# Kernel optimization log

Hardware: AMD Instinct MI355X
Metric: run time of the kernel (lower is better)

The kernel has to match this reference:

```python
import jax, jax.numpy as jnp
import numpy as np

B, N, D, H = 256, 64, 128, 64

def _w(key, shape, fan_in):
    return jax.random.normal(key, shape, jnp.float32) * (1.0 / np.sqrt(fan_in))

def setup_inputs() -> dict:
    key = jax.random.key(0)
    ks = jax.random.split(key, 6)
    return {
        "observations": jax.random.normal(ks[0], (B, N, D), jnp.float32),
        "enc_w": _w(ks[1], (D, H), D), "enc_b": jnp.zeros((H,), jnp.float32),
        "gate_w1": _w(ks[2], (2 * H, H), 2 * H), "gate_b1": jnp.zeros((H,), jnp.float32),
        "gate_w2": _w(ks[3], (H, 1), H), "gate_b2": jnp.zeros((1,), jnp.float32),
        "msg_w1": _w(ks[4], (H, H), H), "msg_b1": jnp.zeros((H,), jnp.float32),
        "msg_w2": _w(ks[5], (H, H), H), "msg_b2": jnp.zeros((H,), jnp.float32),
    }

def reference(observations, enc_w, enc_b, gate_w1, gate_b1, gate_w2, gate_b2,
              msg_w1, msg_b1, msg_w2, msg_b2):
    # encoder: (B, N, H)
    enc = jax.nn.relu(observations @ enc_w + enc_b)
    h = enc.shape[-1]
    # gate layer 1 on concat([e_i, e_j]) == e_i @ W_top + e_j @ W_bot; avoids
    # materializing the (B, N, N, 2H) concat tensor.
    w_i, w_j = gate_w1[:h], gate_w1[h:]
    gi = enc @ w_i                       # (B, N, H) contribution of receiver i
    gj = enc @ w_j + gate_b1             # (B, N, H) contribution of sender j
    hid = jax.nn.relu(gi[:, :, None, :] + gj[:, None, :, :])   # (B, N, N, H)
    gates = jax.nn.sigmoid(jnp.squeeze(hid @ gate_w2, -1) + gate_b2[0])  # (B, N, N)
    # message_gen(encoded): identical for every i in the original loop
    msg = jax.nn.relu(enc @ msg_w1 + msg_b1) @ msg_w2 + msg_b2  # (B, N, H)
    # enhanced[b, i] = sum_j gates[b, i, j] * msg[b, j]
    enhanced = jnp.einsum('bij,bjh->bih', gates, msg)           # (B, N, H)
    return enhanced
```

## Files before the change

### kernel.cpp

```cpp
#include <hip/hip_runtime.h>

typedef float  f32x4  __attribute__((ext_vector_type(4)));
typedef short  bf16x8 __attribute__((ext_vector_type(8)));

#define Bb 256

__device__ __forceinline__ uint cvtpk(float lo, float hi) {
    uint r;
    asm("v_cvt_pk_bf16_f32 %0, %1, %2" : "=v"(r) : "v"(lo), "v"(hi));
    return r;
}
__device__ __forceinline__ ushort f2b1(float v) { return (ushort)cvtpk(v, v); }

__device__ __forceinline__ void gl_lds16(const void* g, void* l) {
    __builtin_amdgcn_global_load_lds(
        (const __attribute__((address_space(1))) unsigned int*)g,
        (__attribute__((address_space(3))) unsigned int*)l, 16, 0, 0);
}

union U8 { uint u[4]; bf16x8 v; };

__global__ __launch_bounds__(256) void gcm_prep(
    const float* __restrict__ obs, const float* __restrict__ enc_w,
    const float* __restrict__ gate_w1, const float* __restrict__ msg_w1,
    const float* __restrict__ msg_w2,
    ushort* __restrict__ obs_bf, ushort* __restrict__ wimg)
{
    const int bid = blockIdx.x, t = threadIdx.x;
    if (bid < 1024) {
        const int G  = bid * 256 + t;
        const int e0 = G * 8;
        const int b  = e0 >> 13;
        const int r  = (e0 >> 7) & 63;
        const int d0 = e0 & 127;
        const int ds = d0 ^ ((r & 7) << 3);
        const float* src = obs + (((size_t)b * 64 + r) * 128 + ds);
        float4 f0 = *(const float4*)src;
        float4 f1 = *(const float4*)(src + 4);
        uint4 o;
        o.x = cvtpk(f0.x, f0.y); o.y = cvtpk(f0.z, f0.w);
        o.z = cvtpk(f1.x, f1.y); o.w = cvtpk(f1.z, f1.w);
        *(uint4*)(obs_bf + e0) = o;
    } else {
        const int G  = (bid - 1024) * 256 + t;
        const int e0 = G * 8;
        float v[8];
        if (e0 < 8192) {
            const int n  = e0 >> 7;
            const int k0 = (e0 & 127) ^ ((n & 7) << 3);
            #pragma unroll
            for (int j = 0; j < 8; ++j) v[j] = enc_w[(k0 + j) * 64 + n];
        } else {
            const int e  = e0 - 8192;
            const int n  = e >> 6;
            const int k0 = (e & 63) ^ ((n & 7) << 3);
            const float* base; int col;
            if (n < 64)       { base = gate_w1;           col = n;       }
            else if (n < 128) { base = gate_w1 + 64 * 64; col = n - 64;  }
            else if (n < 192) { base = msg_w1;            col = n - 128; }
            else              { base = msg_w2;            col = n - 192; }
            #pragma unroll
            for (int j = 0; j < 8; ++j) v[j] = base[(k0 + j) * 64 + col];
        }
        uint4 o;
        o.x = cvtpk(v[0], v[1]); o.y = cvtpk(v[2], v[3]);
        o.z = cvtpk(v[4], v[5]); o.w = cvtpk(v[6], v[7]);
        *(uint4*)(wimg + e0) = o;
    }
}

__global__ __launch_bounds__(1024, 1) void gcm_main(
    const ushort* __restrict__ obs_bf, const ushort* __restrict__ wimg,
    const float* __restrict__ enc_b, const float* __restrict__ gate_b1,
    const float* __restrict__ gate_w2, const float* __restrict__ gate_b2,
    const float* __restrict__ msg_b1, const float* __restrict__ msg_b2,
    float* __restrict__ out)
{
    const int bb   = blockIdx.x;
    const int t    = threadIdx.x;
    const int lane = t & 63;
    const int wv   = t >> 6;
    const int lr   = lane & 15;
    const int lg   = lane >> 4;
    const int rt   = wv & 3;
    const int ct   = wv >> 2;

    __shared__ __align__(16) char arena[131072];
    ushort* s_obs    = (ushort*)(arena);
    ushort* s_encwT  = (ushort*)(arena + 16384);
    ushort* s_wT     = (ushort*)(arena + 32768);
    ushort* s_enc    = (ushort*)(arena + 65536);
    ushort* s_msgh   = (ushort*)(arena + 73728);
    float*  s_gi     = (float*) (arena + 81920);
    float*  s_gj     = (float*) (arena + 98304);
    ushort* s_msgT   = (ushort*)(arena + 114688);
    ushort* s_gatesb = (ushort*)(arena + 122880);

    {
        const ushort* ob = obs_bf + (size_t)bb * 8192 + wv * 512 + lane * 8;
        gl_lds16(ob, arena + wv * 1024);
        const ushort* ew = wimg + wv * 512 + lane * 8;
        gl_lds16(ew, arena + 16384 + wv * 1024);
        const ushort* w0 = wimg + 8192 + wv * 512 + lane * 8;
        gl_lds16(w0, arena + 32768 + wv * 1024);
        const ushort* w1 = wimg + 8192 + (wv + 16) * 512 + lane * 8;
        gl_lds16(w1, arena + 32768 + (wv + 16) * 1024);
    }
    __syncthreads();

    {
        f32x4 acc = (f32x4){0.f, 0.f, 0.f, 0.f};
        const int arow = rt * 16 + lr;
        const int n = ct * 16 + lr;
        #pragma unroll
        for (int ks = 0; ks < 4; ++ks) {
            const int k0 = ks * 32 + lg * 8;
            bf16x8 a  = *(const bf16x8*)(s_obs + ((arow * 128 + k0) ^ ((arow & 7) << 3)));
            bf16x8 bf = *(const bf16x8*)(s_encwT + ((n * 128 + k0) ^ ((n & 7) << 3)));
            acc = __builtin_amdgcn_mfma_f32_16x16x32_bf16(a, bf, acc, 0, 0, 0);
        }
        const float be = enc_b[n];
        float v0 = fmaxf(acc[0] + be, 0.f), v1 = fmaxf(acc[1] + be, 0.f);
        float v2 = fmaxf(acc[2] + be, 0.f), v3 = fmaxf(acc[3] + be, 0.f);
        uint pA = cvtpk(v0, v1), pB = cvtpk(v2, v3);
        const int rb = rt * 16 + lg * 4;
        s_enc[((rb + 0) * 64 + n) ^ (((rb + 0) & 7) << 3)] = (ushort)pA;
        s_enc[((rb + 1) * 64 + n) ^ (((rb + 1) & 7) << 3)] = (ushort)(pA >> 16);
        s_enc[((rb + 2) * 64 + n) ^ (((rb + 2) & 7) << 3)] = (ushort)pB;
        s_enc[((rb + 3) * 64 + n) ^ (((rb + 3) & 7) << 3)] = (ushort)(pB >> 16);
    }
    __syncthreads();

    {
        f32x4 acc[3];
        #pragma unroll
        for (int q = 0; q < 3; ++q) acc[q] = (f32x4){0.f, 0.f, 0.f, 0.f};
        const int arow = rt * 16 + lr;
        #pragma unroll
        for (int ks = 0; ks < 2; ++ks) {
            const int k0 = ks * 32 + lg * 8;
            bf16x8 a = *(const bf16x8*)(s_enc + ((arow * 64 + k0) ^ ((arow & 7) << 3)));
            #pragma unroll
            for (int q = 0; q < 3; ++q) {
                const int n = (ct * 3 + q) * 16 + lr;
                bf16x8 bf = *(const bf16x8*)(s_wT + ((n * 64 + k0) ^ ((n & 7) << 3)));
                acc[q] = __builtin_amdgcn_mfma_f32_16x16x32_bf16(a, bf, acc[q], 0, 0, 0);
            }
        }
        const int rb = rt * 16 + lg * 4;
        #pragma unroll
        for (int q = 0; q < 3; ++q) {
            const int nfull = (ct * 3 + q) * 16;
            const int cc = nfull + lr;
            if (nfull < 64) {
                #pragma unroll
                for (int rr = 0; rr < 4; ++rr) {
                    const int row = rb + rr;
                    s_gi[(row * 64 + cc) ^ ((row & 7) << 2)] = acc[q][rr];
                }
            } else if (nfull < 128) {
                const float b1 = gate_b1[cc - 64];
                #pragma unroll
                for (int rr = 0; rr < 4; ++rr) {
                    const int row = rb + rr;
                    s_gj[(row * 64 + (cc - 64)) ^ ((row & 7) << 2)] = acc[q][rr] + b1;
                }
            } else {
                const float bm = msg_b1[cc - 128];
                float v0 = fmaxf(acc[q][0] + bm, 0.f), v1 = fmaxf(acc[q][1] + bm, 0.f);
                float v2 = fmaxf(acc[q][2] + bm, 0.f), v3 = fmaxf(acc[q][3] + bm, 0.f);
                uint pA = cvtpk(v0, v1), pB = cvtpk(v2, v3);
                const int c2 = cc - 128;
                s_msgh[((rb + 0) * 64 + c2) ^ (((rb + 0) & 7) << 3)] = (ushort)pA;
                s_msgh[((rb + 1) * 64 + c2) ^ (((rb + 1) & 7) << 3)] = (ushort)(pA >> 16);
                s_msgh[((rb + 2) * 64 + c2) ^ (((rb + 2) & 7) << 3)] = (ushort)pB;
                s_msgh[((rb + 3) * 64 + c2) ^ (((rb + 3) & 7) << 3)] = (ushort)(pB >> 16);
            }
        }
    }
    __syncthreads();

    {
        f32x4 acc = (f32x4){0.f, 0.f, 0.f, 0.f};
        const int arow = rt * 16 + lr;
        const int nn3 = 192 + ct * 16 + lr;
        #pragma unroll
        for (int ks = 0; ks < 2; ++ks) {
            const int k0 = ks * 32 + lg * 8;
            bf16x8 a  = *(const bf16x8*)(s_msgh + ((arow * 64 + k0) ^ ((arow & 7) << 3)));
            bf16x8 bf = *(const bf16x8*)(s_wT + ((nn3 * 64 + k0) ^ ((nn3 & 7) << 3)));
            acc = __builtin_amdgcn_mfma_f32_16x16x32_bf16(a, bf, acc, 0, 0, 0);
        }
        const int h  = ct * 16 + lr;
        const int jb = rt * 16 + lg * 4;
        const float bm2 = msg_b2[h];
        uint pA = cvtpk(acc[0] + bm2, acc[1] + bm2);
        uint pB = cvtpk(acc[2] + bm2, acc[3] + bm2);
        const int e = (h * 64 + jb) ^ ((h & 7) << 3);
        *(uint*)(s_msgT + e)     = pA;
        *(uint*)(s_msgT + e + 2) = pB;
    }

    {
        const int row0g = wv * 4;
        float ag[4] = {0.f, 0.f, 0.f, 0.f};
        #pragma unroll 4
        for (int h0 = 0; h0 < 64; h0 += 4) {
            float4 gj4 = *(const float4*)&s_gj[(lane * 64 + h0) ^ ((lane & 7) << 2)];
            const float4 w24 = *(const float4*)(gate_w2 + h0);
            #pragma unroll
            for (int r = 0; r < 4; ++r) {
                const int row = row0g + r;
                float4 gi4 = *(const float4*)&s_gi[(row * 64 + h0) ^ ((row & 7) << 2)];
                ag[r] = fmaf(fmaxf(gi4.x + gj4.x, 0.f), w24.x, ag[r]);
                ag[r] = fmaf(fmaxf(gi4.y + gj4.y, 0.f), w24.y, ag[r]);
                ag[r] = fmaf(fmaxf(gi4.z + gj4.z, 0.f), w24.z, ag[r]);
                ag[r] = fmaf(fmaxf(gi4.w + gj4.w, 0.f), w24.w, ag[r]);
            }
        }
        const float b2v = gate_b2[0];
        #pragma unroll
        for (int r = 0; r < 4; ++r) {
            const int row = row0g + r;
            const float g = 1.f / (1.f + __expf(-(ag[r] + b2v)));
            s_gatesb[(row * 64 + lane) ^ ((row & 7) << 3)] = f2b1(g);
        }
    }
    __syncthreads();

    {
        const int rtl = wv >> 2;
        const int ctl = wv & 3;
        f32x4 acc = (f32x4){0.f, 0.f, 0.f, 0.f};
        const int arow = rtl * 16 + lr;
        const int n = ctl * 16 + lr;
        #pragma unroll
        for (int ks = 0; ks < 2; ++ks) {
            const int k0 = ks * 32 + lg * 8;
            bf16x8 a  = *(const bf16x8*)(s_gatesb + ((arow * 64 + k0) ^ ((arow & 7) << 3)));
            bf16x8 bf = *(const bf16x8*)(s_msgT   + ((n * 64 + k0) ^ ((n & 7) << 3)));
            acc = __builtin_amdgcn_mfma_f32_16x16x32_bf16(a, bf, acc, 0, 0, 0);
        }
        const int rb = rtl * 16 + lg * 4;
        #pragma unroll
        for (int rr = 0; rr < 4; ++rr)
            out[((size_t)bb * 64 + rb + rr) * 64 + n] = acc[rr];
    }
}

__global__ __launch_bounds__(1024) void gcm_fb(
    const float* __restrict__ obs, const float* __restrict__ enc_w,
    const float* __restrict__ enc_b, const float* __restrict__ gate_w1,
    const float* __restrict__ gate_b1, const float* __restrict__ gate_w2,
    const float* __restrict__ gate_b2, const float* __restrict__ msg_w1,
    const float* __restrict__ msg_b1, const float* __restrict__ msg_w2,
    const float* __restrict__ msg_b2, float* __restrict__ out)
{
    const int bb   = blockIdx.x;
    const int t    = threadIdx.x;
    const int lane = t & 63;
    const int wv   = t >> 6;
    const int lr   = lane & 15;
    const int lg   = lane >> 4;
    const int rt   = wv & 3;
    const int ct   = wv >> 2;

    __shared__ __align__(16) ushort s_encwT[64 * 128];
    __shared__ __align__(16) ushort s_wT[256 * 64];
    __shared__ __align__(16) ushort s_enc[64 * 64];
    __shared__ __align__(16) ushort s_msgh[64 * 64];
    __shared__ __align__(16) ushort s_gatesb[64 * 64];
    __shared__ __align__(16) ushort s_msgT[64 * 64];
    __shared__ __align__(16) float  s_gi[64 * 64];
    __shared__ __align__(16) float  s_gj[64 * 64];
    __shared__ __align__(16) float  s_w2[64];

    float4 pf[8];
    {
        const float* ob = obs + ((size_t)bb * 64 + rt * 16 + lr) * 128 + lg * 8;
        #pragma unroll
        for (int ks = 0; ks < 4; ++ks) {
            pf[2 * ks]     = *(const float4*)(ob + ks * 32);
            pf[2 * ks + 1] = *(const float4*)(ob + ks * 32 + 4);
        }
    }
    if (t < 64) s_w2[t] = gate_w2[t];
    #pragma unroll
    for (int it = 0; it < 2; ++it) {
        const int g  = t + it * 1024;
        const int k  = g >> 4;
        const int n0 = (g & 15) * 4;
        float4 w4 = *(const float4*)(enc_w + k * 64 + n0);
        uint pA = cvtpk(w4.x, w4.y), pB = cvtpk(w4.z, w4.w);
        s_encwT[((n0 + 0) * 128 + k) ^ (((n0 + 0) & 7) << 3)] = (ushort)pA;
        s_encwT[((n0 + 1) * 128 + k) ^ (((n0 + 1) & 7) << 3)] = (ushort)(pA >> 16);
        s_encwT[((n0 + 2) * 128 + k) ^ (((n0 + 2) & 7) << 3)] = (ushort)pB;
        s_encwT[((n0 + 3) * 128 + k) ^ (((n0 + 3) & 7) << 3)] = (ushort)(pB >> 16);
    }
    bf16x8 afrag[4];
    #pragma unroll
    for (int ks = 0; ks < 4; ++ks) {
        U8 u;
        u.u[0] = cvtpk(pf[2 * ks].x,     pf[2 * ks].y);
        u.u[1] = cvtpk(pf[2 * ks].z,     pf[2 * ks].w);
        u.u[2] = cvtpk(pf[2 * ks + 1].x, pf[2 * ks + 1].y);
        u.u[3] = cvtpk(pf[2 * ks + 1].z, pf[2 * ks + 1].w);
        afrag[ks] = u.v;
    }
    float4 pfw[4];
    {
        const int k  = t >> 4;
        const int n0 = (t & 15) * 4;
        pfw[0] = *(const float4*)(gate_w1 + k * 64 + n0);
        pfw[1] = *(const float4*)(gate_w1 + (64 + k) * 64 + n0);
        pfw[2] = *(const float4*)(msg_w1 + k * 64 + n0);
        pfw[3] = *(const float4*)(msg_w2 + k * 64 + n0);
    }
    __syncthreads();
    {
        f32x4 acc = (f32x4){0.f, 0.f, 0.f, 0.f};
        const int n = ct * 16 + lr;
        #pragma unroll
        for (int ks = 0; ks < 4; ++ks) {
            const int k0 = ks * 32 + lg * 8;
            bf16x8 bf = *(const bf16x8*)(s_encwT + ((n * 128 + k0) ^ ((n & 7) << 3)));
            acc = __builtin_amdgcn_mfma_f32_16x16x32_bf16(afrag[ks], bf, acc, 0, 0, 0);
        }
        #pragma unroll
        for (int it = 0; it < 4; ++it) {
            const int k  = t >> 4;
            const int n0 = it * 64 + (t & 15) * 4;
            uint pA = cvtpk(pfw[it].x, pfw[it].y), pB = cvtpk(pfw[it].z, pfw[it].w);
            s_wT[((n0 + 0) * 64 + k) ^ (((n0 + 0) & 7) << 3)] = (ushort)pA;
            s_wT[((n0 + 1) * 64 + k) ^ (((n0 + 1) & 7) << 3)] = (ushort)(pA >> 16);
            s_wT[((n0 + 2) * 64 + k) ^ (((n0 + 2) & 7) << 3)] = (ushort)pB;
            s_wT[((n0 + 3) * 64 + k) ^ (((n0 + 3) & 7) << 3)] = (ushort)(pB >> 16);
        }
        const float be = enc_b[n];
        float v0 = fmaxf(acc[0] + be, 0.f), v1 = fmaxf(acc[1] + be, 0.f);
        float v2 = fmaxf(acc[2] + be, 0.f), v3 = fmaxf(acc[3] + be, 0.f);
        uint pA = cvtpk(v0, v1), pB = cvtpk(v2, v3);
        const int rb = rt * 16 + lg * 4;
        s_enc[((rb + 0) * 64 + n) ^ (((rb + 0) & 7) << 3)] = (ushort)pA;
        s_enc[((rb + 1) * 64 + n) ^ (((rb + 1) & 7) << 3)] = (ushort)(pA >> 16);
        s_enc[((rb + 2) * 64 + n) ^ (((rb + 2) & 7) << 3)] = (ushort)pB;
        s_enc[((rb + 3) * 64 + n) ^ (((rb + 3) & 7) << 3)] = (ushort)(pB >> 16);
    }
    __syncthreads();
    {
        f32x4 acc[3];
        #pragma unroll
        for (int q = 0; q < 3; ++q) acc[q] = (f32x4){0.f, 0.f, 0.f, 0.f};
        const int arow = rt * 16 + lr;
        #pragma unroll
        for (int ks = 0; ks < 2; ++ks) {
            const int k0 = ks * 32 + lg * 8;
            bf16x8 a = *(const bf16x8*)(s_enc + ((arow * 64 + k0) ^ ((arow & 7) << 3)));
            #pragma unroll
            for (int q = 0; q < 3; ++q) {
                const int n = (ct * 3 + q) * 16 + lr;
                bf16x8 bf = *(const bf16x8*)(s_wT + ((n * 64 + k0) ^ ((n & 7) << 3)));
                acc[q] = __builtin_amdgcn_mfma_f32_16x16x32_bf16(a, bf, acc[q], 0, 0, 0);
            }
        }
        const int rb = rt * 16 + lg * 4;
        #pragma unroll
        for (int q = 0; q < 3; ++q) {
            const int nfull = (ct * 3 + q) * 16;
            const int cc = nfull + lr;
            if (nfull < 64) {
                #pragma unroll
                for (int rr = 0; rr < 4; ++rr) {
                    const int row = rb + rr;
                    s_gi[(row * 64 + cc) ^ ((row & 7) << 2)] = acc[q][rr];
                }
            } else if (nfull < 128) {
                const float b1 = gate_b1[cc - 64];
                #pragma unroll
                for (int rr = 0; rr < 4; ++rr) {
                    const int row = rb + rr;
                    s_gj[(row * 64 + (cc - 64)) ^ ((row & 7) << 2)] = acc[q][rr] + b1;
                }
            } else {
                const float bm = msg_b1[cc - 128];
                float v0 = fmaxf(acc[q][0] + bm, 0.f), v1 = fmaxf(acc[q][1] + bm, 0.f);
                float v2 = fmaxf(acc[q][2] + bm, 0.f), v3 = fmaxf(acc[q][3] + bm, 0.f);
                uint pA = cvtpk(v0, v1), pB = cvtpk(v2, v3);
                const int c2 = cc - 128;
                s_msgh[((rb + 0) * 64 + c2) ^ (((rb + 0) & 7) << 3)] = (ushort)pA;
                s_msgh[((rb + 1) * 64 + c2) ^ (((rb + 1) & 7) << 3)] = (ushort)(pA >> 16);
                s_msgh[((rb + 2) * 64 + c2) ^ (((rb + 2) & 7) << 3)] = (ushort)pB;
                s_msgh[((rb + 3) * 64 + c2) ^ (((rb + 3) & 7) << 3)] = (ushort)(pB >> 16);
            }
        }
    }
    __syncthreads();
    {
        f32x4 acc = (f32x4){0.f, 0.f, 0.f, 0.f};
        const int arow = rt * 16 + lr;
        const int nn3 = 192 + ct * 16 + lr;
        #pragma unroll
        for (int ks = 0; ks < 2; ++ks) {
            const int k0 = ks * 32 + lg * 8;
            bf16x8 a = *(const bf16x8*)(s_msgh + ((arow * 64 + k0) ^ ((arow & 7) << 3)));
            bf16x8 bf = *(const bf16x8*)(s_wT + ((nn3 * 64 + k0) ^ ((nn3 & 7) << 3)));
            acc = __builtin_amdgcn_mfma_f32_16x16x32_bf16(a, bf, acc, 0, 0, 0);
        }
        const int h  = ct * 16 + lr;
        const int jb = rt * 16 + lg * 4;
        const float bm2 = msg_b2[h];
        uint pA = cvtpk(acc[0] + bm2, acc[1] + bm2);
        uint pB = cvtpk(acc[2] + bm2, acc[3] + bm2);
        const int e = (h * 64 + jb) ^ ((h & 7) << 3);
        *(uint*)(s_msgT + e)     = pA;
        *(uint*)(s_msgT + e + 2) = pB;
    }
    {
        const int row0g = wv * 4;
        float ag[4] = {0.f, 0.f, 0.f, 0.f};
        #pragma unroll 4
        for (int h0 = 0; h0 < 64; h0 += 4) {
            float4 gj4 = *(const float4*)&s_gj[(lane * 64 + h0) ^ ((lane & 7) << 2)];
            float4 w24 = *(const float4*)&s_w2[h0];
            #pragma unroll
            for (int r = 0; r < 4; ++r) {
                const int row = row0g + r;
                float4 gi4 = *(const float4*)&s_gi[(row * 64 + h0) ^ ((row & 7) << 2)];
                ag[r] = fmaf(fmaxf(gi4.x + gj4.x, 0.f), w24.x, ag[r]);
                ag[r] = fmaf(fmaxf(gi4.y + gj4.y, 0.f), w24.y, ag[r]);
                ag[r] = fmaf(fmaxf(gi4.z + gj4.z, 0.f), w24.z, ag[r]);
                ag[r] = fmaf(fmaxf(gi4.w + gj4.w, 0.f), w24.w, ag[r]);
            }
        }
        const float b2v = gate_b2[0];
        #pragma unroll
        for (int r = 0; r < 4; ++r) {
            const int row = row0g + r;
            const float g = 1.f / (1.f + __expf(-(ag[r] + b2v)));
            s_gatesb[(row * 64 + lane) ^ ((row & 7) << 3)] = f2b1(g);
        }
    }
    __syncthreads();
    {
        const int rtl = wv >> 2;
        const int ctl = wv & 3;
        f32x4 acc = (f32x4){0.f, 0.f, 0.f, 0.f};
        const int arow = rtl * 16 + lr;
        const int n = ctl * 16 + lr;
        #pragma unroll
        for (int ks = 0; ks < 2; ++ks) {
            const int k0 = ks * 32 + lg * 8;
            bf16x8 a  = *(const bf16x8*)(s_gatesb + ((arow * 64 + k0) ^ ((arow & 7) << 3)));
            bf16x8 bf = *(const bf16x8*)(s_msgT   + ((n * 64 + k0) ^ ((n & 7) << 3)));
            acc = __builtin_amdgcn_mfma_f32_16x16x32_bf16(a, bf, acc, 0, 0, 0);
        }
        const int rb = rtl * 16 + lg * 4;
        #pragma unroll
        for (int rr = 0; rr < 4; ++rr)
            out[((size_t)bb * 64 + rb + rr) * 64 + n] = acc[rr];
    }
}

extern "C" void kernel_launch(void* const* d_in, const int* in_sizes, int n_in,
                              void* d_out, int out_size, void* d_ws, size_t ws_size,
                              hipStream_t stream) {
    const float* obs     = (const float*)d_in[0];
    const float* enc_w   = (const float*)d_in[1];
    const float* enc_b   = (const float*)d_in[2];
    const float* gate_w1 = (const float*)d_in[3];
    const float* gate_b1 = (const float*)d_in[4];
    const float* gate_w2 = (const float*)d_in[5];
    const float* gate_b2 = (const float*)d_in[6];
    const float* msg_w1  = (const float*)d_in[7];
    const float* msg_b1  = (const float*)d_in[8];
    const float* msg_w2  = (const float*)d_in[9];
    const float* msg_b2  = (const float*)d_in[10];
    float* out = (float*)d_out;

    const size_t obs_elems = (size_t)Bb * 64 * 128;
    const size_t w_elems   = 24576;
    const size_t need = (obs_elems + w_elems) * sizeof(ushort);
    if (ws_size >= need) {
        ushort* obs_bf = (ushort*)d_ws;
        ushort* wimg   = obs_bf + obs_elems;
        gcm_prep<<<1036, 256, 0, stream>>>(obs, enc_w, gate_w1, msg_w1, msg_w2,
                                           obs_bf, wimg);
        gcm_main<<<Bb, 1024, 0, stream>>>(obs_bf, wimg, enc_b, gate_b1,
                                          gate_w2, gate_b2, msg_b1, msg_b2, out);
    } else {
        gcm_fb<<<Bb, 1024, 0, stream>>>(obs, enc_w, enc_b, gate_w1, gate_b1,
                                        gate_w2, gate_b2, msg_w1, msg_b1,
                                        msg_w2, msg_b2, out);
    }
}
```

Before: 21.61 us.

## Split fused per-batch kernel into two half-row kernels via workspace intermediates

```diff
diff --git a/kernel.cpp b/kernel.cpp
--- a/kernel.cpp
+++ b/kernel.cpp
@@ -11,6 +11,8 @@
     return r;
 }
 __device__ __forceinline__ ushort f2b1(float v) { return (ushort)cvtpk(v, v); }
+__device__ __forceinline__ float bflo(uint u) { return __uint_as_float(u << 16); }
+__device__ __forceinline__ float bfhi(uint u) { return __uint_as_float(u & 0xffff0000u); }
 
 __device__ __forceinline__ void gl_lds16(const void* g, void* l) {
     __builtin_amdgcn_global_load_lds(
@@ -69,12 +71,214 @@
     }
 }
 
-__global__ __launch_bounds__(1024, 1) void gcm_main(
+__global__ __launch_bounds__(512, 4) void gcm_ka(
     const ushort* __restrict__ obs_bf, const ushort* __restrict__ wimg,
     const float* __restrict__ enc_b, const float* __restrict__ gate_b1,
+    const float* __restrict__ msg_b1, const float* __restrict__ msg_b2,
+    ushort* __restrict__ gi_ws, ushort* __restrict__ gj_ws,
+    ushort* __restrict__ msgT_ws)
+{
+    const int bid = blockIdx.x;
+    const int bb  = bid >> 1;
+    const int hR  = bid & 1;
+    const int t    = threadIdx.x;
+    const int lane = t & 63;
+    const int wv   = t >> 6;
+    const int lr   = lane & 15;
+    const int lg   = lane >> 4;
+    const int rt   = wv >> 2;
+    const int ct   = wv & 3;
+
+    __shared__ __align__(16) char arena[65536];
+    ushort* s_obs   = (ushort*)(arena);
+    ushort* s_encwT = (ushort*)(arena + 8192);
+    ushort* s_wT    = (ushort*)(arena + 24576);
+    ushort* s_enc   = (ushort*)(arena + 57344);
+    ushort* s_msgh  = (ushort*)(arena + 61440);
+
+    {
+        const ushort* ob = obs_bf + (size_t)bb * 8192 + hR * 4096 + wv * 512 + lane * 8;
+        gl_lds16(ob, arena + wv * 1024);
+        #pragma unroll
+        for (int i = 0; i < 2; ++i) {
+            const int idx = wv * 2 + i;
+            gl_lds16(wimg + idx * 512 + lane * 8, arena + 8192 + idx * 1024);
+        }
+        #pragma unroll
+        for (int i = 0; i < 4; ++i) {
+            const int idx = wv * 4 + i;
+            gl_lds16(wimg + 8192 + idx * 512 + lane * 8, arena + 24576 + idx * 1024);
+        }
+    }
+    __syncthreads();
+
+    {
+        f32x4 acc = (f32x4){0.f, 0.f, 0.f, 0.f};
+        const int arow = rt * 16 + lr;
+        const int n = ct * 16 + lr;
+        #pragma unroll
+        for (int ks = 0; ks < 4; ++ks) {
+            const int k0 = ks * 32 + lg * 8;
+            bf16x8 a  = *(const bf16x8*)(s_obs + ((arow * 128 + k0) ^ ((arow & 7) << 3)));
+            bf16x8 bf = *(const bf16x8*)(s_encwT + ((n * 128 + k0) ^ ((n & 7) << 3)));
+            acc = __builtin_amdgcn_mfma_f32_16x16x32_bf16(a, bf, acc, 0, 0, 0);
+        }
+        const float be = enc_b[n];
+        float v0 = fmaxf(acc[0] + be, 0.f), v1 = fmaxf(acc[1] + be, 0.f);
+        float v2 = fmaxf(acc[2] + be, 0.f), v3 = fmaxf(acc[3] + be, 0.f);
+        uint pA = cvtpk(v0, v1), pB = cvtpk(v2, v3);
+        const int rb = rt * 16 + lg * 4;
+        s_enc[((rb + 0) * 64 + n) ^ (((rb + 0) & 7) << 3)] = (ushort)pA;
+        s_enc[((rb + 1) * 64 + n) ^ (((rb + 1) & 7) << 3)] = (ushort)(pA >> 16);
+        s_enc[((rb + 2) * 64 + n) ^ (((rb + 2) & 7) << 3)] = (ushort)pB;
+        s_enc[((rb + 3) * 64 + n) ^ (((rb + 3) & 7) << 3)] = (ushort)(pB >> 16);
+    }
+    __syncthreads();
+
+    {
+        f32x4 acc[3];
+        #pragma unroll
+        for (int q = 0; q < 3; ++q) acc[q] = (f32x4){0.f, 0.f, 0.f, 0.f};
+        const int arow = rt * 16 + lr;
+        #pragma unroll
+        for (int ks = 0; ks < 2; ++ks) {
+            const int k0 = ks * 32 + lg * 8;
+            bf16x8 a = *(const bf16x8*)(s_enc + ((arow * 64 + k0) ^ ((arow & 7) << 3)));
+            #pragma unroll
+            for (int q = 0; q < 3; ++q) {
+                const int n = (ct * 3 + q) * 16 + lr;
+                bf16x8 bf = *(const bf16x8*)(s_wT + ((n * 64 + k0) ^ ((n & 7) << 3)));
+                acc[q] = __builtin_amdgcn_mfma_f32_16x16x32_bf16(a, bf, acc[q], 0, 0, 0);
+            }
+        }
+        const int rb = rt * 16 + lg * 4;
+        #pragma unroll
+        for (int q = 0; q < 3; ++q) {
+            const int nfull = (ct * 3 + q) * 16;
+            const int cc = nfull + lr;
+            if (nfull < 64) {
+                #pragma unroll
+                for (int rr = 0; rr < 4; ++rr)
+                    gi_ws[(size_t)bb * 4096 + (hR * 32 + rb + rr) * 64 + cc] = f2b1(acc[q][rr]);
+            } else if (nfull < 128) {
+                const float b1 = gate_b1[cc - 64];
+                #pragma unroll
+                for (int rr = 0; rr < 4; ++rr)
+                    gj_ws[(size_t)bb * 4096 + (hR * 32 + rb + rr) * 64 + (cc - 64)] = f2b1(acc[q][rr] + b1);
+            } else {
+                const float bm = msg_b1[cc - 128];
+                float v0 = fmaxf(acc[q][0] + bm, 0.f), v1 = fmaxf(acc[q][1] + bm, 0.f);
+                float v2 = fmaxf(acc[q][2] + bm, 0.f), v3 = fmaxf(acc[q][3] + bm, 0.f);
+                uint pA = cvtpk(v0, v1), pB = cvtpk(v2, v3);
+                const int c2 = cc - 128;
+                s_msgh[((rb + 0) * 64 + c2) ^ (((rb + 0) & 7) << 3)] = (ushort)pA;
+                s_msgh[((rb + 1) * 64 + c2) ^ (((rb + 1) & 7) << 3)] = (ushort)(pA >> 16);
+                s_msgh[((rb + 2) * 64 + c2) ^ (((rb + 2) & 7) << 3)] = (ushort)pB;
+                s_msgh[((rb + 3) * 64 + c2) ^ (((rb + 3) & 7) << 3)] = (ushort)(pB >> 16);
+            }
+        }
+    }
+    __syncthreads();
+
+    {
+        f32x4 acc = (f32x4){0.f, 0.f, 0.f, 0.f};
+        const int arow = rt * 16 + lr;
+        const int nn3 = 192 + ct * 16 + lr;
+        #pragma unroll
+        for (int ks = 0; ks < 2; ++ks) {
+            const int k0 = ks * 32 + lg * 8;
+            bf16x8 a  = *(const bf16x8*)(s_msgh + ((arow * 64 + k0) ^ ((arow & 7) << 3)));
+            bf16x8 bf = *(const bf16x8*)(s_wT + ((nn3 * 64 + k0) ^ ((nn3 & 7) << 3)));
+            acc = __builtin_amdgcn_mfma_f32_16x16x32_bf16(a, bf, acc, 0, 0, 0);
+        }
+        const int h  = ct * 16 + lr;
+        const int jg = hR * 32 + rt * 16 + lg * 4;
+        const float bm2 = msg_b2[h];
+        uint pA = cvtpk(acc[0] + bm2, acc[1] + bm2);
+        uint pB = cvtpk(acc[2] + bm2, acc[3] + bm2);
+        const int e = (h * 64 + jg) ^ ((h & 7) << 3);
+        *(uint*)(msgT_ws + (size_t)bb * 4096 + e)     = pA;
+        *(uint*)(msgT_ws + (size_t)bb * 4096 + e + 2) = pB;
+    }
+}
+
+__global__ __launch_bounds__(512, 4) void gcm_kb(
     const float* __restrict__ gate_w2, const float* __restrict__ gate_b2,
-    const float* __restrict__ msg_b1, const float* __restrict__ msg_b2,
-    float* __restrict__ out)
+    const ushort* __restrict__ gi_ws, const ushort* __restrict__ gj_ws,
+    const ushort* __restrict__ msgT_ws, float* __restrict__ out)
+{
+    const int bid = blockIdx.x;
+    const int bb  = bid >> 1;
+    const int hR  = bid & 1;
+    const int t    = threadIdx.x;
+    const int lane = t & 63;
+    const int wv   = t >> 6;
+    const int lr   = lane & 15;
+    const int lg   = lane >> 4;
+
+    __shared__ __align__(16) char karena[12288];
+    ushort* s_msgT   = (ushort*)(karena);
+    ushort* s_gatesb = (ushort*)(karena + 8192);
+
+    gl_lds16(msgT_ws + (size_t)bb * 4096 + wv * 512 + lane * 8, karena + wv * 1024);
+
+    float gjv[64];
+    {
+        const ushort* gp = gj_ws + (size_t)bb * 4096 + lane * 64;
+        #pragma unroll
+        for (int c = 0; c < 8; ++c) {
+            uint4 p = *(const uint4*)(gp + c * 8);
+            gjv[c * 8 + 0] = bflo(p.x); gjv[c * 8 + 1] = bfhi(p.x);
+            gjv[c * 8 + 2] = bflo(p.y); gjv[c * 8 + 3] = bfhi(p.y);
+            gjv[c * 8 + 4] = bflo(p.z); gjv[c * 8 + 5] = bfhi(p.z);
+            gjv[c * 8 + 6] = bflo(p.w); gjv[c * 8 + 7] = bfhi(p.w);
+        }
+    }
+    const float b2v = gate_b2[0];
+
+    #pragma unroll
+    for (int r = 0; r < 4; ++r) {
+        const int lrow = wv * 4 + r;
+        const int grow = __builtin_amdgcn_readfirstlane(hR * 32 + lrow);
+        const uint* gip = (const uint*)(gi_ws + (size_t)bb * 4096 + grow * 64);
+        float acc = 0.f;
+        #pragma unroll
+        for (int c = 0; c < 32; ++c) {
+            const uint p = gip[c];
+            acc = fmaf(fmaxf(bflo(p) + gjv[2 * c],     0.f), gate_w2[2 * c],     acc);
+            acc = fmaf(fmaxf(bfhi(p) + gjv[2 * c + 1], 0.f), gate_w2[2 * c + 1], acc);
+        }
+        const float g = 1.f / (1.f + __expf(-(acc + b2v)));
+        s_gatesb[(lrow * 64 + lane) ^ ((lrow & 7) << 3)] = f2b1(g);
+    }
+    __syncthreads();
+
+    {
+        const int rtl = wv >> 2, ctl = wv & 3;
+        f32x4 acc = (f32x4){0.f, 0.f, 0.f, 0.f};
+        const int arow = rtl * 16 + lr;
+        const int n = ctl * 16 + lr;
+        #pragma unroll
+        for (int ks = 0; ks < 2; ++ks) {
+            const int k0 = ks * 32 + lg * 8;
+            bf16x8 a  = *(const bf16x8*)(s_gatesb + ((arow * 64 + k0) ^ ((arow & 7) << 3)));
+            bf16x8 bf = *(const bf16x8*)(s_msgT   + ((n * 64 + k0) ^ ((n & 7) << 3)));
+            acc = __builtin_amdgcn_mfma_f32_16x16x32_bf16(a, bf, acc, 0, 0, 0);
+        }
+        const int rb = hR * 32 + rtl * 16 + lg * 4;
+        #pragma unroll
+        for (int rr = 0; rr < 4; ++rr)
+            out[((size_t)bb * 64 + rb + rr) * 64 + n] = acc[rr];
+    }
+}
+
+__global__ __launch_bounds__(1024) void gcm_fb(
+    const float* __restrict__ obs, const float* __restrict__ enc_w,
+    const float* __restrict__ enc_b, const float* __restrict__ gate_w1,
+    const float* __restrict__ gate_b1, const float* __restrict__ gate_w2,
+    const float* __restrict__ gate_b2, const float* __restrict__ msg_w1,
+    const float* __restrict__ msg_b1, const float* __restrict__ msg_w2,
+    const float* __restrict__ msg_b2, float* __restrict__ out)
 {
     const int bb   = blockIdx.x;
     const int t    = threadIdx.x;
@@ -85,39 +289,76 @@
     const int rt   = wv & 3;
     const int ct   = wv >> 2;
 
-    __shared__ __align__(16) char arena[131072];
-    ushort* s_obs    = (ushort*)(arena);
-    ushort* s_encwT  = (ushort*)(arena + 16384);
-    ushort* s_wT     = (ushort*)(arena + 32768);
-    ushort* s_enc    = (ushort*)(arena + 65536);
-    ushort* s_msgh   = (ushort*)(arena + 73728);
-    float*  s_gi     = (float*) (arena + 81920);
-    float*  s_gj     = (float*) (arena + 98304);
-    ushort* s_msgT   = (ushort*)(arena + 114688);
-    ushort* s_gatesb = (ushort*)(arena + 122880);
-
-    {
-        const ushort* ob = obs_bf + (size_t)bb * 8192 + wv * 512 + lane * 8;
-        gl_lds16(ob, arena + wv * 1024);
-        const ushort* ew = wimg + wv * 512 + lane * 8;
-        gl_lds16(ew, arena + 16384 + wv * 1024);
-        const ushort* w0 = wimg + 8192 + wv * 512 + lane * 8;
-        gl_lds16(w0, arena + 32768 + wv * 1024);
-        const ushort* w1 = wimg + 8192 + (wv + 16) * 512 + lane * 8;
-        gl_lds16(w1, arena + 32768 + (wv + 16) * 1024);
-    }
-    __syncthreads();
-
+    __shared__ __align__(16) ushort s_encwT[64 * 128];
+    __shared__ __align__(16) ushort s_wT[256 * 64];
+    __shared__ __align__(16) ushort s_enc[64 * 64];
+    __shared__ __align__(16) ushort s_msgh[64 * 64];
+    __shared__ __align__(16) ushort s_gatesb[64 * 64];
+    __shared__ __align__(16) ushort s_msgT[64 * 64];
+    __shared__ __align__(16) float  s_gi[64 * 64];
+    __shared__ __align__(16) float  s_gj[64 * 64];
+    __shared__ __align__(16) float  s_w2[64];
+
+    float4 pf[8];
+    {
+        const float* ob = obs + ((size_t)bb * 64 + rt * 16 + lr) * 128 + lg * 8;
+        #pragma unroll
+        for (int ks = 0; ks < 4; ++ks) {
+            pf[2 * ks]     = *(const float4*)(ob + ks * 32);
+            pf[2 * ks + 1] = *(const float4*)(ob + ks * 32 + 4);
+        }
+    }
+    if (t < 64) s_w2[t] = gate_w2[t];
+    #pragma unroll
+    for (int it = 0; it < 2; ++it) {
+        const int g  = t + it * 1024;
+        const int k  = g >> 4;
+        const int n0 = (g & 15) * 4;
+        float4 w4 = *(const float4*)(enc_w + k * 64 + n0);
+        uint pA = cvtpk(w4.x, w4.y), pB = cvtpk(w4.z, w4.w);
+        s_encwT[((n0 + 0) * 128 + k) ^ (((n0 + 0) & 7) << 3)] = (ushort)pA;
+        s_encwT[((n0 + 1) * 128 + k) ^ (((n0 + 1) & 7) << 3)] = (ushort)(pA >> 16);
+        s_encwT[((n0 + 2) * 128 + k) ^ (((n0 + 2) & 7) << 3)] = (ushort)pB;
+        s_encwT[((n0 + 3) * 128 + k) ^ (((n0 + 3) & 7) << 3)] = (ushort)(pB >> 16);
+    }
+    bf16x8 afrag[4];
+    #pragma unroll
+    for (int ks = 0; ks < 4; ++ks) {
+        U8 u;
+        u.u[0] = cvtpk(pf[2 * ks].x,     pf[2 * ks].y);
+        u.u[1] = cvtpk(pf[2 * ks].z,     pf[2 * ks].w);
+        u.u[2] = cvtpk(pf[2 * ks + 1].x, pf[2 * ks + 1].y);
+        u.u[3] = cvtpk(pf[2 * ks + 1].z, pf[2 * ks + 1].w);
+        afrag[ks] = u.v;
+    }
+    float4 pfw[4];
+    {
+        const int k  = t >> 4;
+        const int n0 = (t & 15) * 4;
+        pfw[0] = *(const float4*)(gate_w1 + k * 64 + n0);
+        pfw[1] = *(const float4*)(gate_w1 + (64 + k) * 64 + n0);
+        pfw[2] = *(const float4*)(msg_w1 + k * 64 + n0);
+        pfw[3] = *(const float4*)(msg_w2 + k * 64 + n0);
+    }
+    __syncthreads();
     {
         f32x4 acc = (f32x4){0.f, 0.f, 0.f, 0.f};
-        const int arow = rt * 16 + lr;
         const int n = ct * 16 + lr;
         #pragma unroll
         for (int ks = 0; ks < 4; ++ks) {
             const int k0 = ks * 32 + lg * 8;
-            bf16x8 a  = *(const bf16x8*)(s_obs + ((arow * 128 + k0) ^ ((arow & 7) << 3)));
             bf16x8 bf = *(const bf16x8*)(s_encwT + ((n * 128 + k0) ^ ((n & 7) << 3)));
-            acc = __builtin_amdgcn_mfma_f32_16x16x32_bf16(a, bf, acc, 0, 0, 0);
+            acc = __builtin_amdgcn_mfma_f32_16x16x32_bf16(afrag[ks], bf, acc, 0, 0, 0);
+        }
+        #pragma unroll
+        for (int it = 0; it < 4; ++it) {
+            const int k  = t >> 4;
+            const int n0 = it * 64 + (t & 15) * 4;
+            uint pA = cvtpk(pfw[it].x, pfw[it].y), pB = cvtpk(pfw[it].z, pfw[it].w);
+            s_wT[((n0 + 0) * 64 + k) ^ (((n0 + 0) & 7) << 3)] = (ushort)pA;
+            s_wT[((n0 + 1) * 64 + k) ^ (((n0 + 1) & 7) << 3)] = (ushort)(pA >> 16);
+            s_wT[((n0 + 2) * 64 + k) ^ (((n0 + 2) & 7) << 3)] = (ushort)pB;
+            s_wT[((n0 + 3) * 64 + k) ^ (((n0 + 3) & 7) << 3)] = (ushort)(pB >> 16);
         }
         const float be = enc_b[n];
         float v0 = fmaxf(acc[0] + be, 0.f), v1 = fmaxf(acc[1] + be, 0.f);
@@ -130,7 +371,6 @@
         s_enc[((rb + 3) * 64 + n) ^ (((rb + 3) & 7) << 3)] = (ushort)(pB >> 16);
     }
     __syncthreads();
-
     {
         f32x4 acc[3];
         #pragma unroll
@@ -179,222 +419,6 @@
         }
     }
     __syncthreads();
-
-    {
-        f32x4 acc = (f32x4){0.f, 0.f, 0.f, 0.f};
-        const int arow = rt * 16 + lr;
-        const int nn3 = 192 + ct * 16 + lr;
-        #pragma unroll
-        for (int ks = 0; ks < 2; ++ks) {
-            const int k0 = ks * 32 + lg * 8;
-            bf16x8 a  = *(const bf16x8*)(s_msgh + ((arow * 64 + k0) ^ ((arow & 7) << 3)));
-            bf16x8 bf = *(const bf16x8*)(s_wT + ((nn3 * 64 + k0) ^ ((nn3 & 7) << 3)));
-            acc = __builtin_amdgcn_mfma_f32_16x16x32_bf16(a, bf, acc, 0, 0, 0);
-        }
-        const int h  = ct * 16 + lr;
-        const int jb = rt * 16 + lg * 4;
-        const float bm2 = msg_b2[h];
-        uint pA = cvtpk(acc[0] + bm2, acc[1] + bm2);
-        uint pB = cvtpk(acc[2] + bm2, acc[3] + bm2);
-        const int e = (h * 64 + jb) ^ ((h & 7) << 3);
-        *(uint*)(s_msgT + e)     = pA;
-        *(uint*)(s_msgT + e + 2) = pB;
-    }
-
-    {
-        const int row0g = wv * 4;
-        float ag[4] = {0.f, 0.f, 0.f, 0.f};
-        #pragma unroll 4
-        for (int h0 = 0; h0 < 64; h0 += 4) {
-            float4 gj4 = *(const float4*)&s_gj[(lane * 64 + h0) ^ ((lane & 7) << 2)];
-            const float4 w24 = *(const float4*)(gate_w2 + h0);
-            #pragma unroll
-            for (int r = 0; r < 4; ++r) {
-                const int row = row0g + r;
-                float4 gi4 = *(const float4*)&s_gi[(row * 64 + h0) ^ ((row & 7) << 2)];
-                ag[r] = fmaf(fmaxf(gi4.x + gj4.x, 0.f), w24.x, ag[r]);
-                ag[r] = fmaf(fmaxf(gi4.y + gj4.y, 0.f), w24.y, ag[r]);
-                ag[r] = fmaf(fmaxf(gi4.z + gj4.z, 0.f), w24.z, ag[r]);
-                ag[r] = fmaf(fmaxf(gi4.w + gj4.w, 0.f), w24.w, ag[r]);
-            }
-        }
-        const float b2v = gate_b2[0];
-        #pragma unroll
-        for (int r = 0; r < 4; ++r) {
-            const int row = row0g + r;
-            const float g = 1.f / (1.f + __expf(-(ag[r] + b2v)));
-            s_gatesb[(row * 64 + lane) ^ ((row & 7) << 3)] = f2b1(g);
-        }
-    }
-    __syncthreads();
-
-    {
-        const int rtl = wv >> 2;
-        const int ctl = wv & 3;
-        f32x4 acc = (f32x4){0.f, 0.f, 0.f, 0.f};
-        const int arow = rtl * 16 + lr;
-        const int n = ctl * 16 + lr;
-        #pragma unroll
-        for (int ks = 0; ks < 2; ++ks) {
-            const int k0 = ks * 32 + lg * 8;
-            bf16x8 a  = *(const bf16x8*)(s_gatesb + ((arow * 64 + k0) ^ ((arow & 7) << 3)));
-            bf16x8 bf = *(const bf16x8*)(s_msgT   + ((n * 64 + k0) ^ ((n & 7) << 3)));
-            acc = __builtin_amdgcn_mfma_f32_16x16x32_bf16(a, bf, acc, 0, 0, 0);
-        }
-        const int rb = rtl * 16 + lg * 4;
-        #pragma unroll
-        for (int rr = 0; rr < 4; ++rr)
-            out[((size_t)bb * 64 + rb + rr) * 64 + n] = acc[rr];
-    }
-}
-
-__global__ __launch_bounds__(1024) void gcm_fb(
-    const float* __restrict__ obs, const float* __restrict__ enc_w,
-    const float* __restrict__ enc_b, const float* __restrict__ gate_w1,
-    const float* __restrict__ gate_b1, const float* __restrict__ gate_w2,
-    const float* __restrict__ gate_b2, const float* __restrict__ msg_w1,
-    const float* __restrict__ msg_b1, const float* __restrict__ msg_w2,
-    const float* __restrict__ msg_b2, float* __restrict__ out)
-{
-    const int bb   = blockIdx.x;
-    const int t    = threadIdx.x;
-    const int lane = t & 63;
-    const int wv   = t >> 6;
-    const int lr   = lane & 15;
-    const int lg   = lane >> 4;
-    const int rt   = wv & 3;
-    const int ct   = wv >> 2;
-
-    __shared__ __align__(16) ushort s_encwT[64 * 128];
-    __shared__ __align__(16) ushort s_wT[256 * 64];
-    __shared__ __align__(16) ushort s_enc[64 * 64];
-    __shared__ __align__(16) ushort s_msgh[64 * 64];
-    __shared__ __align__(16) ushort s_gatesb[64 * 64];
-    __shared__ __align__(16) ushort s_msgT[64 * 64];
-    __shared__ __align__(16) float  s_gi[64 * 64];
-    __shared__ __align__(16) float  s_gj[64 * 64];
-    __shared__ __align__(16) float  s_w2[64];
-
-    float4 pf[8];
-    {
-        const float* ob = obs + ((size_t)bb * 64 + rt * 16 + lr) * 128 + lg * 8;
-        #pragma unroll
-        for (int ks = 0; ks < 4; ++ks) {
-            pf[2 * ks]     = *(const float4*)(ob + ks * 32);
-            pf[2 * ks + 1] = *(const float4*)(ob + ks * 32 + 4);
-        }
-    }
-    if (t < 64) s_w2[t] = gate_w2[t];
-    #pragma unroll
-    for (int it = 0; it < 2; ++it) {
-        const int g  = t + it * 1024;
-        const int k  = g >> 4;
-        const int n0 = (g & 15) * 4;
-        float4 w4 = *(const float4*)(enc_w + k * 64 + n0);
-        uint pA = cvtpk(w4.x, w4.y), pB = cvtpk(w4.z, w4.w);
-        s_encwT[((n0 + 0) * 128 + k) ^ (((n0 + 0) & 7) << 3)] = (ushort)pA;
-        s_encwT[((n0 + 1) * 128 + k) ^ (((n0 + 1) & 7) << 3)] = (ushort)(pA >> 16);
-        s_encwT[((n0 + 2) * 128 + k) ^ (((n0 + 2) & 7) << 3)] = (ushort)pB;
-        s_encwT[((n0 + 3) * 128 + k) ^ (((n0 + 3) & 7) << 3)] = (ushort)(pB >> 16);
-    }
-    bf16x8 afrag[4];
-    #pragma unroll
-    for (int ks = 0; ks < 4; ++ks) {
-        U8 u;
-        u.u[0] = cvtpk(pf[2 * ks].x,     pf[2 * ks].y);
-        u.u[1] = cvtpk(pf[2 * ks].z,     pf[2 * ks].w);
-        u.u[2] = cvtpk(pf[2 * ks + 1].x, pf[2 * ks + 1].y);
-        u.u[3] = cvtpk(pf[2 * ks + 1].z, pf[2 * ks + 1].w);
-        afrag[ks] = u.v;
-    }
-    float4 pfw[4];
-    {
-        const int k  = t >> 4;
-        const int n0 = (t & 15) * 4;
-        pfw[0] = *(const float4*)(gate_w1 + k * 64 + n0);
-        pfw[1] = *(const float4*)(gate_w1 + (64 + k) * 64 + n0);
-        pfw[2] = *(const float4*)(msg_w1 + k * 64 + n0);
-        pfw[3] = *(const float4*)(msg_w2 + k * 64 + n0);
-    }
-    __syncthreads();
-    {
-        f32x4 acc = (f32x4){0.f, 0.f, 0.f, 0.f};
-        const int n = ct * 16 + lr;
-        #pragma unroll
-        for (int ks = 0; ks < 4; ++ks) {
-            const int k0 = ks * 32 + lg * 8;
-            bf16x8 bf = *(const bf16x8*)(s_encwT + ((n * 128 + k0) ^ ((n & 7) << 3)));
-            acc = __builtin_amdgcn_mfma_f32_16x16x32_bf16(afrag[ks], bf, acc, 0, 0, 0);
-        }
-        #pragma unroll
-        for (int it = 0; it < 4; ++it) {
-            const int k  = t >> 4;
-            const int n0 = it * 64 + (t & 15) * 4;
-            uint pA = cvtpk(pfw[it].x, pfw[it].y), pB = cvtpk(pfw[it].z, pfw[it].w);
-            s_wT[((n0 + 0) * 64 + k) ^ (((n0 + 0) & 7) << 3)] = (ushort)pA;
-            s_wT[((n0 + 1) * 64 + k) ^ (((n0 + 1) & 7) << 3)] = (ushort)(pA >> 16);
-            s_wT[((n0 + 2) * 64 + k) ^ (((n0 + 2) & 7) << 3)] = (ushort)pB;
-            s_wT[((n0 + 3) * 64 + k) ^ (((n0 + 3) & 7) << 3)] = (ushort)(pB >> 16);
-        }
-        const float be = enc_b[n];
-        float v0 = fmaxf(acc[0] + be, 0.f), v1 = fmaxf(acc[1] + be, 0.f);
-        float v2 = fmaxf(acc[2] + be, 0.f), v3 = fmaxf(acc[3] + be, 0.f);
-        uint pA = cvtpk(v0, v1), pB = cvtpk(v2, v3);
-        const int rb = rt * 16 + lg * 4;
-        s_enc[((rb + 0) * 64 + n) ^ (((rb + 0) & 7) << 3)] = (ushort)pA;
-        s_enc[((rb + 1) * 64 + n) ^ (((rb + 1) & 7) << 3)] = (ushort)(pA >> 16);
-        s_enc[((rb + 2) * 64 + n) ^ (((rb + 2) & 7) << 3)] = (ushort)pB;
-        s_enc[((rb + 3) * 64 + n) ^ (((rb + 3) & 7) << 3)] = (ushort)(pB >> 16);
-    }
-    __syncthreads();
-    {
-        f32x4 acc[3];
-        #pragma unroll
-        for (int q = 0; q < 3; ++q) acc[q] = (f32x4){0.f, 0.f, 0.f, 0.f};
-        const int arow = rt * 16 + lr;
-        #pragma unroll
-        for (int ks = 0; ks < 2; ++ks) {
-            const int k0 = ks * 32 + lg * 8;
-            bf16x8 a = *(const bf16x8*)(s_enc + ((arow * 64 + k0) ^ ((arow & 7) << 3)));
-            #pragma unroll
-            for (int q = 0; q < 3; ++q) {
-                const int n = (ct * 3 + q) * 16 + lr;
-                bf16x8 bf = *(const bf16x8*)(s_wT + ((n * 64 + k0) ^ ((n & 7) << 3)));
-                acc[q] = __builtin_amdgcn_mfma_f32_16x16x32_bf16(a, bf, acc[q], 0, 0, 0);
-            }
-        }
-        const int rb = rt * 16 + lg * 4;
-        #pragma unroll
-        for (int q = 0; q < 3; ++q) {
-            const int nfull = (ct * 3 + q) * 16;
-            const int cc = nfull + lr;
-            if (nfull < 64) {
-                #pragma unroll
-                for (int rr = 0; rr < 4; ++rr) {
-                    const int row = rb + rr;
-                    s_gi[(row * 64 + cc) ^ ((row & 7) << 2)] = acc[q][rr];
-                }
-            } else if (nfull < 128) {
-                const float b1 = gate_b1[cc - 64];
-                #pragma unroll
-                for (int rr = 0; rr < 4; ++rr) {
-                    const int row = rb + rr;
-                    s_gj[(row * 64 + (cc - 64)) ^ ((row & 7) << 2)] = acc[q][rr] + b1;
-                }
-            } else {
-                const float bm = msg_b1[cc - 128];
-                float v0 = fmaxf(acc[q][0] + bm, 0.f), v1 = fmaxf(acc[q][1] + bm, 0.f);
-                float v2 = fmaxf(acc[q][2] + bm, 0.f), v3 = fmaxf(acc[q][3] + bm, 0.f);
-                uint pA = cvtpk(v0, v1), pB = cvtpk(v2, v3);
-                const int c2 = cc - 128;
-                s_msgh[((rb + 0) * 64 + c2) ^ (((rb + 0) & 7) << 3)] = (ushort)pA;
-                s_msgh[((rb + 1) * 64 + c2) ^ (((rb + 1) & 7) << 3)] = (ushort)(pA >> 16);
-                s_msgh[((rb + 2) * 64 + c2) ^ (((rb + 2) & 7) << 3)] = (ushort)pB;
-                s_msgh[((rb + 3) * 64 + c2) ^ (((rb + 3) & 7) << 3)] = (ushort)(pB >> 16);
-            }
-        }
-    }
-    __syncthreads();
     {
         f32x4 acc = (f32x4){0.f, 0.f, 0.f, 0.f};
         const int arow = rt * 16 + lr;
@@ -479,14 +503,20 @@
 
     const size_t obs_elems = (size_t)Bb * 64 * 128;
     const size_t w_elems   = 24576;
-    const size_t need = (obs_elems + w_elems) * sizeof(ushort);
+    const size_t per       = (size_t)Bb * 64 * 64;
+    const size_t need = (obs_elems + w_elems + 3 * per) * sizeof(ushort);
     if (ws_size >= need) {
-        ushort* obs_bf = (ushort*)d_ws;
-        ushort* wimg   = obs_bf + obs_elems;
+        ushort* obs_bf  = (ushort*)d_ws;
+        ushort* wimg    = obs_bf + obs_elems;
+        ushort* gi_ws   = wimg + w_elems;
+        ushort* gj_ws   = gi_ws + per;
+        ushort* msgT_ws = gj_ws + per;
         gcm_prep<<<1036, 256, 0, stream>>>(obs, enc_w, gate_w1, msg_w1, msg_w2,
                                            obs_bf, wimg);
-        gcm_main<<<Bb, 1024, 0, stream>>>(obs_bf, wimg, enc_b, gate_b1,
-                                          gate_w2, gate_b2, msg_b1, msg_b2, out);
+        gcm_ka<<<2 * Bb, 512, 0, stream>>>(obs_bf, wimg, enc_b, gate_b1,
+                                           msg_b1, msg_b2, gi_ws, gj_ws, msgT_ws);
+        gcm_kb<<<2 * Bb, 512, 0, stream>>>(gate_w2, gate_b2, gi_ws, gj_ws,
+                                           msgT_ws, out);
     } else {
         gcm_fb<<<Bb, 1024, 0, stream>>>(obs, enc_w, enc_b, gate_w1, gate_b1,
                                         gate_w2, gate_b2, msg_w1, msg_b1,
```

After: 27.16 us. 1.26x slower.
